# Kernel optimization log

Measured on AMD Instinct MI355X. Metric: run time of the kernel, lower is better.

Reference implementation:

```python
import jax, jax.numpy as jnp
import numpy as np

BLOCK = 128
FP8_MAX = 448.0


def _quantize_weight_blockwise(w):
    """Blockwise fp8 quantization of weight [O, I] -> (fp8-valued f32 weight, [O/B, I/B] scales)."""
    O, I = w.shape
    wb = w.reshape(O // BLOCK, BLOCK, I // BLOCK, BLOCK)
    amax = jnp.maximum(jnp.max(jnp.abs(wb), axis=(1, 3), keepdims=True), 1e-12)
    scale = amax / FP8_MAX  # [O/B,1,I/B,1]
    w_fp8 = (wb / scale).astype(jnp.float8_e4m3fn).astype(jnp.float32).reshape(O, I)
    return w_fp8, scale[:, 0, :, 0]


def setup_inputs() -> dict:
    key = jax.random.key(0)
    k1, k2 = jax.random.split(key)
    tokens, input_size, output_size = 8192, 4096, 4096
    x = jax.random.normal(k1, (tokens, input_size), dtype=jnp.float32)
    w_hp = jax.random.normal(k2, (output_size, input_size), dtype=jnp.float32) * 0.02
    weight, weight_scale_inv = _quantize_weight_blockwise(w_hp)
    return {"x": x, "weight": weight, "weight_scale_inv": weight_scale_inv}


def reference(x, weight, weight_scale_inv):
    # --- dynamic per-token fp8 quantization of activations ---
    amax = jnp.maximum(jnp.max(jnp.abs(x), axis=-1, keepdims=True), 1e-12)  # [T,1]
    x_scale = amax / FP8_MAX                                                # [T,1] f32
    x_fp8 = (x / x_scale).astype(jnp.float8_e4m3fn).astype(jnp.float32)     # fp8-valued f32
    # --- blockwise dequant of fp8 weight with weight_scale_inv ---
    O, I = weight.shape
    scale_full = jnp.repeat(jnp.repeat(weight_scale_inv, BLOCK, axis=0), BLOCK, axis=1)  # [O,I]
    w_deq = weight * scale_full
    # --- fp8 block-scaled GEMM (dequantized-equivalent math) ---
    y = jnp.einsum('tk,ok->to', x_fp8, w_deq) * x_scale  # [T, O]
    return y
```

## Files before the change

kernel.cpp:

```cpp
#include <hip/hip_runtime.h>
#include <stdint.h>

#define FP8_MAX 448.0f
#define TOKENS  8192
#define IDIM    4096
#define ODIM    4096

typedef float f32x4 __attribute__((ext_vector_type(4)));

__device__ __forceinline__ void async_copy16(const uint8_t* g, uint8_t* l) {
  __builtin_amdgcn_global_load_lds((const __attribute__((address_space(1))) void*)g,
                                   (__attribute__((address_space(3))) void*)l,
                                   16, 0, 0);
}

__global__ __launch_bounds__(256) void quant_x_kernel(
    const float* __restrict__ x, uint8_t* __restrict__ xq, float* __restrict__ xsc) {
  const int row = blockIdx.x;
  const int tid = threadIdx.x;
  const float* xr = x + (size_t)row * IDIM;

  float4 v[4];
  float amax = 0.0f;
  #pragma unroll
  for (int k = 0; k < 4; k++) {
    v[k] = ((const float4*)xr)[tid + k * 256];
    amax = fmaxf(amax, fmaxf(fmaxf(fabsf(v[k].x), fabsf(v[k].y)),
                             fmaxf(fabsf(v[k].z), fabsf(v[k].w))));
  }
  #pragma unroll
  for (int off = 32; off > 0; off >>= 1)
    amax = fmaxf(amax, __shfl_xor(amax, off, 64));

  __shared__ float smax[4];
  if ((tid & 63) == 0) smax[tid >> 6] = amax;
  __syncthreads();
  amax = fmaxf(fmaxf(smax[0], smax[1]), fmaxf(smax[2], smax[3]));
  amax = fmaxf(amax, 1e-12f);
  const float scale = amax / FP8_MAX;
  if (tid == 0) xsc[row] = scale;

  uint32_t* out = (uint32_t*)(xq + (size_t)row * IDIM);
  #pragma unroll
  for (int k = 0; k < 4; k++) {
    float a = v[k].x / scale, b = v[k].y / scale;
    float c = v[k].z / scale, d = v[k].w / scale;
    int p = __builtin_amdgcn_cvt_pk_fp8_f32(a, b, 0, false);
    p = __builtin_amdgcn_cvt_pk_fp8_f32(c, d, p, true);
    out[tid + k * 256] = (uint32_t)p;
  }
}

__global__ __launch_bounds__(256) void conv_w_kernel(
    const float* __restrict__ w, uint8_t* __restrict__ wq) {
  const size_t base = (size_t)blockIdx.x * 4096;
  const int tid = threadIdx.x;
  const float4* wp = (const float4*)(w + base);
  uint32_t* out = (uint32_t*)(wq + base);
  #pragma unroll
  for (int k = 0; k < 4; k++) {
    float4 v = wp[tid + k * 256];
    int p = __builtin_amdgcn_cvt_pk_fp8_f32(v.x, v.y, 0, false);
    p = __builtin_amdgcn_cvt_pk_fp8_f32(v.z, v.w, p, true);
    out[tid + k * 256] = (uint32_t)p;
  }
}

__global__ __launch_bounds__(256) void gemm_fp8_kernel(
    const uint8_t* __restrict__ xq, const uint8_t* __restrict__ wq,
    const float* __restrict__ xsc, const float* __restrict__ wsi,
    float* __restrict__ y) {
  __shared__ uint8_t As[128 * 128];
  __shared__ uint8_t Bs[128 * 128];

  const int tid  = threadIdx.x;
  const int bo   = blockIdx.x & 31;
  const int bt   = blockIdx.x >> 5;
  const int t0   = bt << 7;
  const int o0   = bo << 7;
  const int lane = tid & 63;
  const int wave = tid >> 6;
  const int wr   = (wave >> 1) << 6;
  const int wc   = (wave & 1) << 6;
  const int ln   = lane & 15;
  const int quad = lane >> 4;

  const int rb  = tid >> 3;
  const int cs  = ((tid & 7) ^ (rb & 7)) << 4;
  const int lds = tid << 4;

  f32x4 outer[4][4];
  #pragma unroll
  for (int i = 0; i < 4; i++)
    #pragma unroll
    for (int j = 0; j < 4; j++)
      outer[i][j] = (f32x4)(0.0f);

  const float* wsrow = wsi + bo * 32;

  for (int kb = 0; kb < 32; kb++) {
    const int k0 = kb << 7;
    #pragma unroll
    for (int u = 0; u < 4; u++) {
      async_copy16(xq + ((size_t)(t0 + u * 32 + rb) << 12) + (k0 + cs),
                   As + u * 4096 + lds);
      async_copy16(wq + ((size_t)(o0 + u * 32 + rb) << 12) + (k0 + cs),
                   Bs + u * 4096 + lds);
    }
    __syncthreads();

    f32x4 inner[4][4];
    #pragma unroll
    for (int i = 0; i < 4; i++)
      #pragma unroll
      for (int j = 0; j < 4; j++)
        inner[i][j] = (f32x4)(0.0f);

    #pragma unroll
    for (int ks = 0; ks < 4; ks++) {
      const int ch = ks * 2 + (quad >> 1);
      const int b8 = (quad & 1) << 3;
      long a[4], b[4];
      #pragma unroll
      for (int i = 0; i < 4; i++) {
        const int row = wr + i * 16 + ln;
        a[i] = *(const long*)(As + row * 128 + ((ch ^ (row & 7)) << 4) + b8);
      }
      #pragma unroll
      for (int j = 0; j < 4; j++) {
        const int row = wc + j * 16 + ln;
        b[j] = *(const long*)(Bs + row * 128 + ((ch ^ (row & 7)) << 4) + b8);
      }
      #pragma unroll
      for (int i = 0; i < 4; i++)
        #pragma unroll
        for (int j = 0; j < 4; j++)
          inner[i][j] = __builtin_amdgcn_mfma_f32_16x16x32_fp8_fp8(
              a[i], b[j], inner[i][j], 0, 0, 0);
    }

    const float s = wsrow[kb];
    #pragma unroll
    for (int i = 0; i < 4; i++)
      #pragma unroll
      for (int j = 0; j < 4; j++)
        outer[i][j] += s * inner[i][j];
    __syncthreads();
  }

  #pragma unroll
  for (int i = 0; i < 4; i++) {
    #pragma unroll
    for (int r = 0; r < 4; r++) {
      const int t = t0 + wr + i * 16 + quad * 4 + r;
      const float sc = xsc[t];
      float* yp = y + ((size_t)t << 12) + o0 + wc + ln;
      #pragma unroll
      for (int j = 0; j < 4; j++)
        yp[j * 16] = outer[i][j][r] * sc;
    }
  }
}

extern "C" void kernel_launch(void* const* d_in, const int* in_sizes, int n_in,
                              void* d_out, int out_size, void* d_ws, size_t ws_size,
                              hipStream_t stream) {
  const float* x   = (const float*)d_in[0];
  const float* w   = (const float*)d_in[1];
  const float* wsi = (const float*)d_in[2];
  float* y = (float*)d_out;

  uint8_t* xq = (uint8_t*)d_ws;
  uint8_t* wq = xq + (size_t)TOKENS * IDIM;
  float*  xsc = (float*)(wq + (size_t)ODIM * IDIM);

  quant_x_kernel<<<TOKENS, 256, 0, stream>>>(x, xq, xsc);
  conv_w_kernel<<<((size_t)ODIM * IDIM) / 4096, 256, 0, stream>>>(w, wq);
  gemm_fp8_kernel<<<(TOKENS / 128) * (ODIM / 128), 256, 0, stream>>>(xq, wq, xsc, wsi, y);
}
```

Measured before the change: 497.7 us.

## Use 16x16x128 scaled fp8 MFMA and merge prep kernels into one launch

The GEMM inner loop now issues one 16x16x128 scaled MFMA per output tile per K-block, replacing four 16x16x32 fp8 MFMAs. Each lane loads two 16-byte swizzled LDS chunks instead of four 8-byte loads, with per-lane offsets precomputed outside the K loop. Activation quantization and weight conversion are merged into a single launch to remove one kernel launch. Risk: the operand lane layout of the new MFMA must match the swizzled LDS data, and the neutral scale constant must be correct, or the results are wrong.

```diff
diff --git a/kernel.cpp b/kernel.cpp
--- a/kernel.cpp
+++ b/kernel.cpp
@@ -7,6 +7,8 @@
 #define ODIM    4096
 
 typedef float f32x4 __attribute__((ext_vector_type(4)));
+typedef int   i32x4 __attribute__((ext_vector_type(4)));
+typedef int   i32x8 __attribute__((ext_vector_type(8)));
 
 __device__ __forceinline__ void async_copy16(const uint8_t* g, uint8_t* l) {
   __builtin_amdgcn_global_load_lds((const __attribute__((address_space(1))) void*)g,
@@ -14,55 +16,54 @@
                                    16, 0, 0);
 }
 
-__global__ __launch_bounds__(256) void quant_x_kernel(
-    const float* __restrict__ x, uint8_t* __restrict__ xq, float* __restrict__ xsc) {
-  const int row = blockIdx.x;
+__global__ __launch_bounds__(256) void prep_kernel(
+    const float* __restrict__ x, const float* __restrict__ w,
+    uint8_t* __restrict__ xq, uint8_t* __restrict__ wq, float* __restrict__ xsc) {
   const int tid = threadIdx.x;
-  const float* xr = x + (size_t)row * IDIM;
+  if (blockIdx.x < TOKENS) {
+    const int row = blockIdx.x;
+    const f32x4* xr = (const f32x4*)(x + (size_t)row * IDIM);
 
-  float4 v[4];
-  float amax = 0.0f;
-  #pragma unroll
-  for (int k = 0; k < 4; k++) {
-    v[k] = ((const float4*)xr)[tid + k * 256];
-    amax = fmaxf(amax, fmaxf(fmaxf(fabsf(v[k].x), fabsf(v[k].y)),
-                             fmaxf(fabsf(v[k].z), fabsf(v[k].w))));
-  }
-  #pragma unroll
-  for (int off = 32; off > 0; off >>= 1)
-    amax = fmaxf(amax, __shfl_xor(amax, off, 64));
+    f32x4 v[4];
+    float amax = 0.0f;
+    #pragma unroll
+    for (int k = 0; k < 4; k++) {
+      v[k] = xr[tid + k * 256];
+      amax = fmaxf(amax, fmaxf(fmaxf(fabsf(v[k].x), fabsf(v[k].y)),
+                               fmaxf(fabsf(v[k].z), fabsf(v[k].w))));
+    }
+    #pragma unroll
+    for (int off = 32; off > 0; off >>= 1)
+      amax = fmaxf(amax, __shfl_xor(amax, off, 64));
 
-  __shared__ float smax[4];
-  if ((tid & 63) == 0) smax[tid >> 6] = amax;
-  __syncthreads();
-  amax = fmaxf(fmaxf(smax[0], smax[1]), fmaxf(smax[2], smax[3]));
-  amax = fmaxf(amax, 1e-12f);
-  const float scale = amax / FP8_MAX;
-  if (tid == 0) xsc[row] = scale;
+    __shared__ float smax[4];
+    if ((tid & 63) == 0) smax[tid >> 6] = amax;
+    __syncthreads();
+    amax = fmaxf(fmaxf(smax[0], smax[1]), fmaxf(smax[2], smax[3]));
+    amax = fmaxf(amax, 1e-12f);
+    const float scale = amax / FP8_MAX;
+    if (tid == 0) xsc[row] = scale;
 
-  uint32_t* out = (uint32_t*)(xq + (size_t)row * IDIM);
-  #pragma unroll
-  for (int k = 0; k < 4; k++) {
-    float a = v[k].x / scale, b = v[k].y / scale;
-    float c = v[k].z / scale, d = v[k].w / scale;
-    int p = __builtin_amdgcn_cvt_pk_fp8_f32(a, b, 0, false);
-    p = __builtin_amdgcn_cvt_pk_fp8_f32(c, d, p, true);
-    out[tid + k * 256] = (uint32_t)p;
-  }
-}
-
-__global__ __launch_bounds__(256) void conv_w_kernel(
-    const float* __restrict__ w, uint8_t* __restrict__ wq) {
-  const size_t base = (size_t)blockIdx.x * 4096;
-  const int tid = threadIdx.x;
-  const float4* wp = (const float4*)(w + base);
-  uint32_t* out = (uint32_t*)(wq + base);
-  #pragma unroll
-  for (int k = 0; k < 4; k++) {
-    float4 v = wp[tid + k * 256];
-    int p = __builtin_amdgcn_cvt_pk_fp8_f32(v.x, v.y, 0, false);
-    p = __builtin_amdgcn_cvt_pk_fp8_f32(v.z, v.w, p, true);
-    out[tid + k * 256] = (uint32_t)p;
+    uint32_t* out = (uint32_t*)(xq + (size_t)row * IDIM);
+    #pragma unroll
+    for (int k = 0; k < 4; k++) {
+      float a = v[k].x / scale, b = v[k].y / scale;
+      float c = v[k].z / scale, d = v[k].w / scale;
+      int p = __builtin_amdgcn_cvt_pk_fp8_f32(a, b, 0, false);
+      p = __builtin_amdgcn_cvt_pk_fp8_f32(c, d, p, true);
+      out[tid + k * 256] = (uint32_t)p;
+    }
+  } else {
+    const size_t base = (size_t)(blockIdx.x - TOKENS) * 4096;
+    const f32x4* wp = (const f32x4*)(w + base);
+    uint32_t* out = (uint32_t*)(wq + base);
+    #pragma unroll
+    for (int k = 0; k < 4; k++) {
+      f32x4 v = wp[tid + k * 256];
+      int p = __builtin_amdgcn_cvt_pk_fp8_f32(v.x, v.y, 0, false);
+      p = __builtin_amdgcn_cvt_pk_fp8_f32(v.z, v.w, p, true);
+      out[tid + k * 256] = (uint32_t)p;
+    }
   }
 }
 
@@ -70,8 +71,8 @@
     const uint8_t* __restrict__ xq, const uint8_t* __restrict__ wq,
     const float* __restrict__ xsc, const float* __restrict__ wsi,
     float* __restrict__ y) {
-  __shared__ uint8_t As[128 * 128];
-  __shared__ uint8_t Bs[128 * 128];
+  __shared__ __align__(16) uint8_t As[128 * 128];
+  __shared__ __align__(16) uint8_t Bs[128 * 128];
 
   const int tid  = threadIdx.x;
   const int bo   = blockIdx.x & 31;
@@ -89,6 +90,20 @@
   const int cs  = ((tid & 7) ^ (rb & 7)) << 4;
   const int lds = tid << 4;
 
+  const int c0 = quad << 1;
+  int aoff[4][2], boff[4][2];
+  #pragma unroll
+  for (int i = 0; i < 4; i++) {
+    const int ra = wr + i * 16 + ln;
+    const int sa = ra & 7;
+    aoff[i][0] = ra * 128 + ((c0 ^ sa) << 4);
+    aoff[i][1] = ra * 128 + (((c0 + 1) ^ sa) << 4);
+    const int rb2 = wc + i * 16 + ln;
+    const int sb = rb2 & 7;
+    boff[i][0] = rb2 * 128 + ((c0 ^ sb) << 4);
+    boff[i][1] = rb2 * 128 + (((c0 + 1) ^ sb) << 4);
+  }
+
   f32x4 outer[4][4];
   #pragma unroll
   for (int i = 0; i < 4; i++)
@@ -97,6 +112,8 @@
       outer[i][j] = (f32x4)(0.0f);
 
   const float* wsrow = wsi + bo * 32;
+  const int ident = 0x7f7f7f7f;
+  const f32x4 zero4 = (f32x4)(0.0f);
 
   for (int kb = 0; kb < 32; kb++) {
     const int k0 = kb << 7;
@@ -109,42 +126,29 @@
     }
     __syncthreads();
 
-    f32x4 inner[4][4];
+    i32x8 a[4], b[4];
     #pragma unroll
-    for (int i = 0; i < 4; i++)
-      #pragma unroll
-      for (int j = 0; j < 4; j++)
-        inner[i][j] = (f32x4)(0.0f);
-
+    for (int i = 0; i < 4; i++) {
+      i32x4 lo = *(const i32x4*)(As + aoff[i][0]);
+      i32x4 hi = *(const i32x4*)(As + aoff[i][1]);
+      a[i] = __builtin_shufflevector(lo, hi, 0, 1, 2, 3, 4, 5, 6, 7);
+    }
     #pragma unroll
-    for (int ks = 0; ks < 4; ks++) {
-      const int ch = ks * 2 + (quad >> 1);
-      const int b8 = (quad & 1) << 3;
-      long a[4], b[4];
-      #pragma unroll
-      for (int i = 0; i < 4; i++) {
-        const int row = wr + i * 16 + ln;
-        a[i] = *(const long*)(As + row * 128 + ((ch ^ (row & 7)) << 4) + b8);
-      }
-      #pragma unroll
-      for (int j = 0; j < 4; j++) {
-        const int row = wc + j * 16 + ln;
-        b[j] = *(const long*)(Bs + row * 128 + ((ch ^ (row & 7)) << 4) + b8);
-      }
-      #pragma unroll
-      for (int i = 0; i < 4; i++)
-        #pragma unroll
-        for (int j = 0; j < 4; j++)
-          inner[i][j] = __builtin_amdgcn_mfma_f32_16x16x32_fp8_fp8(
-              a[i], b[j], inner[i][j], 0, 0, 0);
+    for (int j = 0; j < 4; j++) {
+      i32x4 lo = *(const i32x4*)(Bs + boff[j][0]);
+      i32x4 hi = *(const i32x4*)(Bs + boff[j][1]);
+      b[j] = __builtin_shufflevector(lo, hi, 0, 1, 2, 3, 4, 5, 6, 7);
     }
 
     const float s = wsrow[kb];
     #pragma unroll
     for (int i = 0; i < 4; i++)
       #pragma unroll
-      for (int j = 0; j < 4; j++)
-        outer[i][j] += s * inner[i][j];
+      for (int j = 0; j < 4; j++) {
+        f32x4 t = __builtin_amdgcn_mfma_scale_f32_16x16x128_f8f6f4(
+            a[i], b[j], zero4, 0, 0, 0, ident, 0, ident);
+        outer[i][j] += s * t;
+      }
     __syncthreads();
   }
 
@@ -174,7 +178,6 @@
   uint8_t* wq = xq + (size_t)TOKENS * IDIM;
   float*  xsc = (float*)(wq + (size_t)ODIM * IDIM);
 
-  quant_x_kernel<<<TOKENS, 256, 0, stream>>>(x, xq, xsc);
-  conv_w_kernel<<<((size_t)ODIM * IDIM) / 4096, 256, 0, stream>>>(w, wq);
+  prep_kernel<<<TOKENS + ((size_t)ODIM * IDIM) / 4096, 256, 0, stream>>>(x, w, xq, wq, xsc);
   gemm_fp8_kernel<<<(TOKENS / 128) * (ODIM / 128), 256, 0, stream>>>(xq, wq, xsc, wsi, y);
 }
```

New measurement: 424.9 us. 1.17x faster.
